# Performance work log

Measured on AMD Instinct MI355X. Metric: run time of the kernel, lower is better.

## Reference

```python
import jax, jax.numpy as jnp
import numpy as np
from jax import lax

B, PN, NS = 8, 16384, 256
KDIM, HID = 512, 384
HALF = HID // 2
EPS = 1e-5


def setup_inputs() -> dict:
    key = jax.random.key(0)
    ks = jax.random.split(key, 12)
    s = lambda fan: np.float32(1.0 / np.sqrt(fan))
    inp = {
        "p": jax.random.normal(ks[0], (B, PN, 3), jnp.float32),
        "N": NS,
        "patch_feature": jax.random.normal(ks[1], (B, KDIM, 1), jnp.float32),
        # Linear(k_dim, hidden)
        "W_feat": jax.random.normal(ks[2], (KDIM, HID), jnp.float32) * s(KDIM),
        "b_feat": jax.random.normal(ks[3], (HID,), jnp.float32) * s(KDIM),
        # Linear(3, hidden//2)
        "W_coord": jax.random.normal(ks[4], (3, HALF), jnp.float32) * s(3),
        "b_coord": jax.random.normal(ks[5], (HALF,), jnp.float32) * s(3),
        # Conv1d(hidden+hidden//2, hidden, 1) == per-point linear, weight (out,in)
        "W1": jax.random.normal(ks[6], (HID, HID + HALF), jnp.float32) * s(HID + HALF),
        "b1": jax.random.normal(ks[7], (HID,), jnp.float32) * s(HID + HALF),
        "g1": jnp.ones((HID,), jnp.float32),
        "be1": jnp.zeros((HID,), jnp.float32),
        # Conv1d(hidden, hidden, 1)
        "W2": jax.random.normal(ks[8], (HID, HID), jnp.float32) * s(HID),
        "b2": jax.random.normal(ks[9], (HID,), jnp.float32) * s(HID),
        "g2": jnp.ones((HID,), jnp.float32),
        "be2": jnp.zeros((HID,), jnp.float32),
    }
    return inp


def farthest_point_sample(points, k):
    """points: (B, N, C) -> (B, k, C). Deterministic start index 0 per batch."""
    b, n, c = points.shape

    def step(carry, _):
        dist, far = carry
        centroid = jnp.take_along_axis(points, far[:, None, None], axis=1)  # (B,1,C)
        d = jnp.sum((points - centroid) ** 2, axis=-1)                      # (B,N)
        dist = jnp.minimum(dist, d)
        new_far = jnp.argmax(dist, axis=-1)
        return (dist, new_far), far

    init = (jnp.full((b, n), 1e10, points.dtype), jnp.zeros((b,), jnp.int32))
    _, idx = lax.scan(step, init, None, length=k)  # idx: (k, B)
    idx = idx.T                                    # (B, k)
    return jnp.take_along_axis(points, idx[:, :, None], axis=1)  # (B,k,C)


def batchnorm(x, gamma, beta):
    """x: (B, L, C); training-mode BN over (B, L) per channel (biased var)."""
    mean = jnp.mean(x, axis=(0, 1))
    var = jnp.var(x, axis=(0, 1))
    return (x - mean) * lax.rsqrt(var + EPS) * gamma + beta


def reference(p, N, patch_feature, W_feat, b_feat, W_coord, b_coord,
              W1, b1, g1, be1, W2, b2, g2, be2):
    b, pn, _ = p.shape
    global_feat = patch_feature[..., 0] @ W_feat + b_feat          # (B, HID)
    global_feat = jnp.broadcast_to(global_feat[:, None, :], (b, N, HID))
    local_feat = p @ W_coord + b_coord                              # (B, PN, HALF)
    if N != pn:
        local_feat = farthest_point_sample(local_feat, N)           # (B, N, HALF)
    combined = jnp.concatenate([global_feat, local_feat], axis=-1)  # (B, N, HID+HALF)
    h = jnp.einsum("bnc,oc->bno", combined, W1) + b1
    h = jax.nn.relu(batchnorm(h, g1, be1))
    h = jnp.einsum("bnc,oc->bno", h, W2) + b2
    h = jax.nn.relu(batchnorm(h, g2, be2))
    return h  # (B, N, HID)
```

## Files before the change

### kernel.cpp

```cpp
#include <hip/hip_runtime.h>

#define BATCH 8
#define PN    16384
#define NSAMP 256
#define KDIM  512
#define HID   384
#define HALF  192
#define CIN   576
#define ROWS  2048
#define BN_EPS 1e-5f

#define OFF_GF   0
#define OFF_W1T  3072
#define OFF_W2T  224256
#define OFF_IDX  371712
#define OFF_H1   373760
#define OFF_H2   1160192
#define OFF_SUM1 1946624
#define OFF_SQ1  1947008
#define OFF_SUM2 1947392
#define OFF_SQ2  1947776

typedef float v2f __attribute__((ext_vector_type(2)));

__device__ __forceinline__ v2f dist2_pk(v2f qx, v2f qy, v2f qz,
                                        v2f cx, v2f cy, v2f cz) {
  v2f dx, dy, dz, d;
  asm("v_pk_add_f32 %0, %4, %7 neg_lo:[0,1] neg_hi:[0,1]\n\t"
      "v_pk_add_f32 %1, %5, %8 neg_lo:[0,1] neg_hi:[0,1]\n\t"
      "v_pk_add_f32 %2, %6, %9 neg_lo:[0,1] neg_hi:[0,1]\n\t"
      "v_pk_mul_f32 %3, %2, %2\n\t"
      "v_pk_fma_f32 %3, %1, %1, %3\n\t"
      "v_pk_fma_f32 %3, %0, %0, %3"
      : "=&v"(dx), "=&v"(dy), "=&v"(dz), "=&v"(d)
      : "v"(qx), "v"(qy), "v"(qz), "v"(cx), "v"(cy), "v"(cz));
  return d;
}

#define DPP_MAX(v, ctrl)                                                   \
  v = fmaxf(v, __int_as_float(__builtin_amdgcn_update_dpp(                 \
          0, __float_as_int(v), (ctrl), 0xf, 0xf, true)))

__global__ __launch_bounds__(1024) void k_main(const float* p, const float* Wc,
                                               const float* pf, const float* Wf,
                                               const float* bfe, const float* W1,
                                               const float* W2, float* ws) {
  __shared__ float s[KDIM];
  __shared__ float Msh[6];
  __shared__ __align__(16) float redv[2][16];
  __shared__ __align__(16) float4 cslot[2][8];
  __shared__ int widx[2], ncl[2];
  int blk = blockIdx.x, t = threadIdx.x;

  if (blk >= 8) {
    if (blk < 16) {
      for (int sI = (blk - 8) * 1024 + t; sI < HID * CIN; sI += 8192) {
        int o = sI / CIN, c = sI % CIN;
        ws[OFF_W1T + c * HID + o] = W1[sI];
      }
    } else if (blk < 24) {
      for (int sI = (blk - 16) * 1024 + t; sI < HID * HID; sI += 8192) {
        int o = sI / HID, c = sI % HID;
        ws[OFF_W2T + c * HID + o] = W2[sI];
      }
    } else if (blk < 32) {
      int b = blk - 24;
      if (t < KDIM) s[t] = pf[b * KDIM + t];
      __syncthreads();
      if (t < HID) {
        float acc = bfe[t];
        for (int k = 0; k < KDIM; k++) acc = fmaf(s[k], Wf[k * HID + t], acc);
        ws[OFF_GF + b * HID + t] = acc;
      }
    } else {
      for (int i = t; i < 1536; i += 1024) ws[OFF_SUM1 + i] = 0.f;
    }
    return;
  }

  int b = blk;
  int* idx_out = (int*)(ws + OFF_IDX);

  if (t < 64) {
    double g0 = 0, g1 = 0, g2 = 0, g3 = 0, g4 = 0, g5 = 0;
    for (int k = t; k < HALF; k += 64) {
      double w0 = (double)Wc[k];
      double w1 = (double)Wc[HALF + k];
      double w2 = (double)Wc[2 * HALF + k];
      g0 += w0 * w0; g1 += w0 * w1; g2 += w0 * w2;
      g3 += w1 * w1; g4 += w1 * w2; g5 += w2 * w2;
    }
    for (int off = 32; off; off >>= 1) {
      g0 += __shfl_down(g0, off, 64); g1 += __shfl_down(g1, off, 64);
      g2 += __shfl_down(g2, off, 64); g3 += __shfl_down(g3, off, 64);
      g4 += __shfl_down(g4, off, 64); g5 += __shfl_down(g5, off, 64);
    }
    if (t == 0) {
      double l00 = sqrt(g0);
      double l10 = g1 / l00, l20 = g2 / l00;
      double l11 = sqrt(g3 - l10 * l10);
      double l21 = (g4 - l10 * l20) / l11;
      double l22 = sqrt(g5 - l20 * l20 - l21 * l21);
      Msh[0] = (float)l00; Msh[1] = (float)l10; Msh[2] = (float)l20;
      Msh[3] = (float)l11; Msh[4] = (float)l21; Msh[5] = (float)l22;
    }
  }
  __syncthreads();
  float m00 = Msh[0], m10 = Msh[1], m20 = Msh[2];
  float m11 = Msh[3], m21 = Msh[4], m22 = Msh[5];

  const float* pb = p + b * PN * 3;
  v2f qx[8], qy[8], qz[8], dist[8];
#pragma unroll
  for (int j = 0; j < 8; j++) {
    int i0 = ((2 * j) << 10) + t;
    int i1 = i0 + 1024;
    float x0 = pb[i0 * 3], y0 = pb[i0 * 3 + 1], z0 = pb[i0 * 3 + 2];
    float x1 = pb[i1 * 3], y1 = pb[i1 * 3 + 1], z1 = pb[i1 * 3 + 2];
    qx[j] = (v2f){fmaf(m00, x0, fmaf(m10, y0, m20 * z0)),
                  fmaf(m00, x1, fmaf(m10, y1, m20 * z1))};
    qy[j] = (v2f){fmaf(m11, y0, m21 * z0), fmaf(m11, y1, m21 * z1)};
    qz[j] = (v2f){m22 * z0, m22 * z1};
    dist[j] = (v2f){1e10f, 1e10f};
  }

  if (t == 0) {
    widx[1] = 0; ncl[1] = 1;
    cslot[1][0] = make_float4(__int_as_float(0), qx[0].x, qy[0].x, qz[0].x);
    widx[0] = 0x7fffffff; ncl[0] = 0;
  }
  __syncthreads();

  int par = 0;
  for (int k = 0; k < NSAMP; k++) {
    int qb = par ^ 1;
    int far = widx[qb];
    float4 s0 = cslot[qb][0];
    float cx = s0.y, cy = s0.z, cz = s0.w;
    if (__float_as_int(s0.x) != far) {
      int n = ncl[qb];
      bool found = false;
      int nn = n < 8 ? n : 8;
      for (int i2 = 1; i2 < nn; i2++) {
        float4 si = cslot[qb][i2];
        if (__float_as_int(si.x) == far) {
          cx = si.y; cy = si.z; cz = si.w; found = true;
        }
      }
      if (!found) {
        float x = pb[far * 3], y = pb[far * 3 + 1], z = pb[far * 3 + 2];
        cx = fmaf(m00, x, fmaf(m10, y, m20 * z));
        cy = fmaf(m11, y, m21 * z);
        cz = m22 * z;
      }
    }
    if (t == 0) {
      idx_out[b * NSAMP + k] = far;
      widx[par] = 0x7fffffff;
      ncl[par] = 0;
    }

    v2f cxv = (v2f){cx, cx}, cyv = (v2f){cy, cy}, czv = (v2f){cz, cz};
#pragma unroll
    for (int j = 0; j < 8; j++) {
      v2f d = dist2_pk(qx[j], qy[j], qz[j], cxv, cyv, czv);
      dist[j].x = fminf(dist[j].x, d.x);
      dist[j].y = fminf(dist[j].y, d.y);
    }
    float a0 = fmaxf(dist[0].x, dist[0].y);
    float a1 = fmaxf(dist[1].x, dist[1].y);
    float a2 = fmaxf(dist[2].x, dist[2].y);
    float a3 = fmaxf(dist[3].x, dist[3].y);
    float a4 = fmaxf(dist[4].x, dist[4].y);
    float a5 = fmaxf(dist[5].x, dist[5].y);
    float a6 = fmaxf(dist[6].x, dist[6].y);
    float a7 = fmaxf(dist[7].x, dist[7].y);
    float b0 = fmaxf(fmaxf(a0, a1), a2);
    float b1 = fmaxf(fmaxf(a3, a4), a5);
    float tmax = fmaxf(fmaxf(b0, b1), fmaxf(a6, a7));
    float wv = tmax;
    DPP_MAX(wv, 0x111);
    DPP_MAX(wv, 0x112);
    DPP_MAX(wv, 0x114);
    DPP_MAX(wv, 0x118);
    DPP_MAX(wv, 0x142);
    DPP_MAX(wv, 0x143);
    if ((t & 63) == 63) redv[par][t >> 6] = wv;
    __syncthreads();
    float4 r0 = *(const float4*)&redv[par][0];
    float4 r1 = *(const float4*)&redv[par][4];
    float4 r2 = *(const float4*)&redv[par][8];
    float4 r3 = *(const float4*)&redv[par][12];
    float g01 = fmaxf(fmaxf(r0.x, r0.y), r0.z);
    float g02 = fmaxf(fmaxf(r0.w, r1.x), r1.y);
    float g03 = fmaxf(fmaxf(r1.z, r1.w), r2.x);
    float g04 = fmaxf(fmaxf(r2.y, r2.z), r2.w);
    float g05 = fmaxf(fmaxf(r3.x, r3.y), r3.z);
    float gmax = fmaxf(fmaxf(fmaxf(g01, g02), g03),
                       fmaxf(fmaxf(g04, g05), r3.w));
    if (tmax == gmax) {
      int mi = 0x7fffffff; float wx = 0.f, wy = 0.f, wz = 0.f;
#pragma unroll
      for (int j = 7; j >= 0; j--) {
        int i0 = ((2 * j) << 10) + t;
        bool hy = (dist[j].y == gmax);
        mi = hy ? i0 + 1024 : mi;
        wx = hy ? qx[j].y : wx; wy = hy ? qy[j].y : wy; wz = hy ? qz[j].y : wz;
        bool hx = (dist[j].x == gmax);
        mi = hx ? i0 : mi;
        wx = hx ? qx[j].x : wx; wy = hx ? qy[j].x : wy; wz = hx ? qz[j].x : wz;
      }
      int pos = atomicAdd(&ncl[par], 1);
      if (pos < 8)
        cslot[par][pos] = make_float4(__int_as_float(mi), wx, wy, wz);
      atomicMin(&widx[par], mi);
    }
    __syncthreads();
    par ^= 1;
  }
}

__global__ __launch_bounds__(384) void k_gemm1(const float* p,
                                               const float* Wc,
                                               const float* bc,
                                               const float* b1,
                                               float* ws) {
  __shared__ __align__(16) float ct[CIN * 8];
  int t = threadIdx.x;
  int row0 = blockIdx.x * 8;
  const int* fidx = (const int*)(ws + OFF_IDX);
  for (int sI = t; sI < 8 * CIN; sI += 384) {
    int r = sI / CIN, c = sI % CIN;
    int row = row0 + r, b = row >> 8;
    float val;
    if (c < HID) {
      val = ws[OFF_GF + b * HID + c];
    } else {
      int co = c - HID;
      int i = fidx[row];
      const float* pp = p + (b * PN + i) * 3;
      val = bc[co];
      val = fmaf(pp[0], Wc[co], val);
      val = fmaf(pp[1], Wc[HALF + co], val);
      val = fmaf(pp[2], Wc[2 * HALF + co], val);
    }
    ct[c * 8 + r] = val;
  }
  __syncthreads();
  const float* w1t = ws + OFF_W1T;
  float acc[8] = {0.f, 0.f, 0.f, 0.f, 0.f, 0.f, 0.f, 0.f};
  for (int c = 0; c < CIN; c++) {
    float w = w1t[c * HID + t];
    float4 a0 = *(const float4*)(ct + c * 8);
    float4 a1 = *(const float4*)(ct + c * 8 + 4);
    acc[0] = fmaf(a0.x, w, acc[0]); acc[1] = fmaf(a0.y, w, acc[1]);
    acc[2] = fmaf(a0.z, w, acc[2]); acc[3] = fmaf(a0.w, w, acc[3]);
    acc[4] = fmaf(a1.x, w, acc[4]); acc[5] = fmaf(a1.y, w, acc[5]);
    acc[6] = fmaf(a1.z, w, acc[6]); acc[7] = fmaf(a1.w, w, acc[7]);
  }
  float bias = b1[t];
  float sv = 0.f, sq = 0.f;
#pragma unroll
  for (int r = 0; r < 8; r++) {
    float v = acc[r] + bias;
    ws[OFF_H1 + (row0 + r) * HID + t] = v;
    sv += v; sq = fmaf(v, v, sq);
  }
  atomicAdd(&ws[OFF_SUM1 + t], sv);
  atomicAdd(&ws[OFF_SQ1 + t], sq);
}

__global__ __launch_bounds__(384) void k_gemm2(const float* b2,
                                               const float* g1,
                                               const float* be1,
                                               float* ws) {
  __shared__ __align__(16) float ht[HID * 8];
  __shared__ float sc1s[HID], sh1s[HID];
  int t = threadIdx.x;
  int row0 = blockIdx.x * 8;
  {
    float m = ws[OFF_SUM1 + t] * (1.f / ROWS);
    float v = ws[OFF_SQ1 + t] * (1.f / ROWS) - m * m;
    float inv = 1.f / sqrtf(v + BN_EPS);
    float sc = inv * g1[t];
    sc1s[t] = sc;
    sh1s[t] = be1[t] - m * sc;
  }
  __syncthreads();
  for (int sI = t; sI < 8 * HID; sI += 384) {
    int r = sI / HID, c = sI % HID;
    float x = fmaf(ws[OFF_H1 + (row0 + r) * HID + c], sc1s[c], sh1s[c]);
    ht[c * 8 + r] = fmaxf(x, 0.f);
  }
  __syncthreads();
  const float* w2t = ws + OFF_W2T;
  float acc[8] = {0.f, 0.f, 0.f, 0.f, 0.f, 0.f, 0.f, 0.f};
  for (int c = 0; c < HID; c++) {
    float w = w2t[c * HID + t];
    float4 a0 = *(const float4*)(ht + c * 8);
    float4 a1 = *(const float4*)(ht + c * 8 + 4);
    acc[0] = fmaf(a0.x, w, acc[0]); acc[1] = fmaf(a0.y, w, acc[1]);
    acc[2] = fmaf(a0.z, w, acc[2]); acc[3] = fmaf(a0.w, w, acc[3]);
    acc[4] = fmaf(a1.x, w, acc[4]); acc[5] = fmaf(a1.y, w, acc[5]);
    acc[6] = fmaf(a1.z, w, acc[6]); acc[7] = fmaf(a1.w, w, acc[7]);
  }
  float bias = b2[t];
  float sv = 0.f, sq = 0.f;
#pragma unroll
  for (int r = 0; r < 8; r++) {
    float v = acc[r] + bias;
    ws[OFF_H2 + (row0 + r) * HID + t] = v;
    sv += v; sq = fmaf(v, v, sq);
  }
  atomicAdd(&ws[OFF_SUM2 + t], sv);
  atomicAdd(&ws[OFF_SQ2 + t], sq);
}

__global__ __launch_bounds__(256) void k_out(const float* ws, const float* g2,
                                             const float* be2, float* out) {
  int gid = blockIdx.x * 256 + threadIdx.x;
  int i = gid * 4;
  int c = i % HID;
  float4 h  = *(const float4*)(ws + OFF_H2 + i);
  float4 s2 = *(const float4*)(ws + OFF_SUM2 + c);
  float4 q2 = *(const float4*)(ws + OFF_SQ2 + c);
  float4 gv = *(const float4*)(g2 + c);
  float4 bv = *(const float4*)(be2 + c);
  float4 r;
#define BN2(comp) {                                                  \
    float m  = s2.comp * (1.f / ROWS);                               \
    float v  = q2.comp * (1.f / ROWS) - m * m;                       \
    float sc = (1.f / sqrtf(v + BN_EPS)) * gv.comp;                  \
    float sh = bv.comp - m * sc;                                     \
    r.comp = fmaxf(fmaf(h.comp, sc, sh), 0.f); }
  BN2(x) BN2(y) BN2(z) BN2(w)
#undef BN2
  ((float4*)out)[gid] = r;
}

extern "C" void kernel_launch(void* const* d_in, const int* in_sizes, int n_in,
                              void* d_out, int out_size, void* d_ws, size_t ws_size,
                              hipStream_t stream) {
  const float* p   = (const float*)d_in[0];
  const float* pf  = (const float*)d_in[2];
  const float* Wf  = (const float*)d_in[3];
  const float* bfe = (const float*)d_in[4];
  const float* Wc  = (const float*)d_in[5];
  const float* bc  = (const float*)d_in[6];
  const float* W1  = (const float*)d_in[7];
  const float* b1  = (const float*)d_in[8];
  const float* g1  = (const float*)d_in[9];
  const float* be1 = (const float*)d_in[10];
  const float* W2  = (const float*)d_in[11];
  const float* b2  = (const float*)d_in[12];
  const float* g2  = (const float*)d_in[13];
  const float* be2 = (const float*)d_in[14];
  float* ws = (float*)d_ws;

  hipLaunchKernelGGL(k_main,  dim3(33),  dim3(1024), 0, stream,
                     p, Wc, pf, Wf, bfe, W1, W2, ws);
  hipLaunchKernelGGL(k_gemm1, dim3(256), dim3(384), 0, stream, p, Wc, bc, b1, ws);
  hipLaunchKernelGGL(k_gemm2, dim3(256), dim3(384), 0, stream, b2, g1, be1, ws);
  hipLaunchKernelGGL(k_out,   dim3(768), dim3(256), 0, stream,
                     ws, g2, be2, (float*)d_out);
}
```

Before: 561.9 us.

## Precompute per-batch global W1 term, expand FPS distance, use shuffle reduction

The global-feature part of the first conv is constant per batch, so it is folded into a per-batch vector (W1_global·gf + b1) computed in k_main. This shrinks the k_gemm1 reduction from 576 to 192 input channels and transposes only the local half of W1. The FPS distance is rewritten as |q|^2+|c|^2-2q·c with precomputed norms, using FMAs instead of subtract-then-square. The DPP wave max becomes a __shfl_xor butterfly. The expanded distance form can change rounding and thus argmax tie-breaking, which risks selecting different points than the reference.

```diff
diff --git a/kernel.cpp b/kernel.cpp
--- a/kernel.cpp
+++ b/kernel.cpp
@@ -12,6 +12,7 @@
 
 #define OFF_GF   0
 #define OFF_W1T  3072
+#define OFF_GFW  76800
 #define OFF_W2T  224256
 #define OFF_IDX  371712
 #define OFF_H1   373760
@@ -23,28 +24,11 @@
 
 typedef float v2f __attribute__((ext_vector_type(2)));
 
-__device__ __forceinline__ v2f dist2_pk(v2f qx, v2f qy, v2f qz,
-                                        v2f cx, v2f cy, v2f cz) {
-  v2f dx, dy, dz, d;
-  asm("v_pk_add_f32 %0, %4, %7 neg_lo:[0,1] neg_hi:[0,1]\n\t"
-      "v_pk_add_f32 %1, %5, %8 neg_lo:[0,1] neg_hi:[0,1]\n\t"
-      "v_pk_add_f32 %2, %6, %9 neg_lo:[0,1] neg_hi:[0,1]\n\t"
-      "v_pk_mul_f32 %3, %2, %2\n\t"
-      "v_pk_fma_f32 %3, %1, %1, %3\n\t"
-      "v_pk_fma_f32 %3, %0, %0, %3"
-      : "=&v"(dx), "=&v"(dy), "=&v"(dz), "=&v"(d)
-      : "v"(qx), "v"(qy), "v"(qz), "v"(cx), "v"(cy), "v"(cz));
-  return d;
-}
-
-#define DPP_MAX(v, ctrl)                                                   \
-  v = fmaxf(v, __int_as_float(__builtin_amdgcn_update_dpp(                 \
-          0, __float_as_int(v), (ctrl), 0xf, 0xf, true)))
-
 __global__ __launch_bounds__(1024) void k_main(const float* p, const float* Wc,
                                                const float* pf, const float* Wf,
                                                const float* bfe, const float* W1,
-                                               const float* W2, float* ws) {
+                                               const float* b1v, const float* W2,
+                                               float* ws) {
   __shared__ float s[KDIM];
   __shared__ float Msh[6];
   __shared__ __align__(16) float redv[2][16];
@@ -54,9 +38,9 @@
 
   if (blk >= 8) {
     if (blk < 16) {
-      for (int sI = (blk - 8) * 1024 + t; sI < HID * CIN; sI += 8192) {
-        int o = sI / CIN, c = sI % CIN;
-        ws[OFF_W1T + c * HID + o] = W1[sI];
+      for (int sI = (blk - 8) * 1024 + t; sI < HID * HALF; sI += 8192) {
+        int o = sI / HALF, c = sI % HALF;
+        ws[OFF_W1T + c * HID + o] = W1[o * CIN + HID + c];
       }
     } else if (blk < 24) {
       for (int sI = (blk - 16) * 1024 + t; sI < HID * HID; sI += 8192) {
@@ -67,10 +51,20 @@
       int b = blk - 24;
       if (t < KDIM) s[t] = pf[b * KDIM + t];
       __syncthreads();
+      float acc = 0.f;
       if (t < HID) {
-        float acc = bfe[t];
+        acc = bfe[t];
         for (int k = 0; k < KDIM; k++) acc = fmaf(s[k], Wf[k * HID + t], acc);
         ws[OFF_GF + b * HID + t] = acc;
+      }
+      __syncthreads();
+      if (t < HID) s[t] = acc;
+      __syncthreads();
+      if (t < HID) {
+        float g = b1v[t];
+        const float* w1row = W1 + t * CIN;
+        for (int c = 0; c < HID; c++) g = fmaf(s[c], w1row[c], g);
+        ws[OFF_GFW + b * HID + t] = g;
       }
     } else {
       for (int i = t; i < 1536; i += 1024) ws[OFF_SUM1 + i] = 0.f;
@@ -110,7 +104,7 @@
   float m11 = Msh[3], m21 = Msh[4], m22 = Msh[5];
 
   const float* pb = p + b * PN * 3;
-  v2f qx[8], qy[8], qz[8], dist[8];
+  v2f qx[8], qy[8], qz[8], nq[8], dist[8];
 #pragma unroll
   for (int j = 0; j < 8; j++) {
     int i0 = ((2 * j) << 10) + t;
@@ -121,6 +115,9 @@
                   fmaf(m00, x1, fmaf(m10, y1, m20 * z1))};
     qy[j] = (v2f){fmaf(m11, y0, m21 * z0), fmaf(m11, y1, m21 * z1)};
     qz[j] = (v2f){m22 * z0, m22 * z1};
+    nq[j] = __builtin_elementwise_fma(
+        qx[j], qx[j],
+        __builtin_elementwise_fma(qy[j], qy[j], qz[j] * qz[j]));
     dist[j] = (v2f){1e10f, 1e10f};
   }
 
@@ -160,10 +157,17 @@
       ncl[par] = 0;
     }
 
-    v2f cxv = (v2f){cx, cx}, cyv = (v2f){cy, cy}, czv = (v2f){cz, cz};
+    float nc = fmaf(cx, cx, fmaf(cy, cy, cz * cz));
+    float cx2 = -2.f * cx, cy2 = -2.f * cy, cz2 = -2.f * cz;
+    v2f cxv = (v2f){cx2, cx2}, cyv = (v2f){cy2, cy2}, czv = (v2f){cz2, cz2};
+    v2f ncv = (v2f){nc, nc};
 #pragma unroll
     for (int j = 0; j < 8; j++) {
-      v2f d = dist2_pk(qx[j], qy[j], qz[j], cxv, cyv, czv);
+      v2f base = nq[j] + ncv;
+      v2f d = __builtin_elementwise_fma(
+          qx[j], cxv,
+          __builtin_elementwise_fma(qy[j], cyv,
+              __builtin_elementwise_fma(qz[j], czv, base)));
       dist[j].x = fminf(dist[j].x, d.x);
       dist[j].y = fminf(dist[j].y, d.y);
     }
@@ -178,14 +182,10 @@
     float b0 = fmaxf(fmaxf(a0, a1), a2);
     float b1 = fmaxf(fmaxf(a3, a4), a5);
     float tmax = fmaxf(fmaxf(b0, b1), fmaxf(a6, a7));
-    float wv = tmax;
-    DPP_MAX(wv, 0x111);
-    DPP_MAX(wv, 0x112);
-    DPP_MAX(wv, 0x114);
-    DPP_MAX(wv, 0x118);
-    DPP_MAX(wv, 0x142);
-    DPP_MAX(wv, 0x143);
-    if ((t & 63) == 63) redv[par][t >> 6] = wv;
+    float m = tmax;
+#pragma unroll
+    for (int off = 32; off; off >>= 1) m = fmaxf(m, __shfl_xor(m, off, 64));
+    if ((t & 63) == 0) redv[par][t >> 6] = m;
     __syncthreads();
     float4 r0 = *(const float4*)&redv[par][0];
     float4 r1 = *(const float4*)&redv[par][4];
@@ -223,33 +223,27 @@
 __global__ __launch_bounds__(384) void k_gemm1(const float* p,
                                                const float* Wc,
                                                const float* bc,
-                                               const float* b1,
                                                float* ws) {
-  __shared__ __align__(16) float ct[CIN * 8];
+  __shared__ __align__(16) float ct[HALF * 8];
   int t = threadIdx.x;
   int row0 = blockIdx.x * 8;
+  int b = row0 >> 8;
   const int* fidx = (const int*)(ws + OFF_IDX);
-  for (int sI = t; sI < 8 * CIN; sI += 384) {
-    int r = sI / CIN, c = sI % CIN;
-    int row = row0 + r, b = row >> 8;
-    float val;
-    if (c < HID) {
-      val = ws[OFF_GF + b * HID + c];
-    } else {
-      int co = c - HID;
-      int i = fidx[row];
-      const float* pp = p + (b * PN + i) * 3;
-      val = bc[co];
-      val = fmaf(pp[0], Wc[co], val);
-      val = fmaf(pp[1], Wc[HALF + co], val);
-      val = fmaf(pp[2], Wc[2 * HALF + co], val);
-    }
-    ct[c * 8 + r] = val;
+  for (int sI = t; sI < 8 * HALF; sI += 384) {
+    int r = sI / HALF, co = sI % HALF;
+    int row = row0 + r;
+    int i = fidx[row];
+    const float* pp = p + (b * PN + i) * 3;
+    float val = bc[co];
+    val = fmaf(pp[0], Wc[co], val);
+    val = fmaf(pp[1], Wc[HALF + co], val);
+    val = fmaf(pp[2], Wc[2 * HALF + co], val);
+    ct[co * 8 + r] = val;
   }
   __syncthreads();
   const float* w1t = ws + OFF_W1T;
   float acc[8] = {0.f, 0.f, 0.f, 0.f, 0.f, 0.f, 0.f, 0.f};
-  for (int c = 0; c < CIN; c++) {
+  for (int c = 0; c < HALF; c++) {
     float w = w1t[c * HID + t];
     float4 a0 = *(const float4*)(ct + c * 8);
     float4 a1 = *(const float4*)(ct + c * 8 + 4);
@@ -258,11 +252,11 @@
     acc[4] = fmaf(a1.x, w, acc[4]); acc[5] = fmaf(a1.y, w, acc[5]);
     acc[6] = fmaf(a1.z, w, acc[6]); acc[7] = fmaf(a1.w, w, acc[7]);
   }
-  float bias = b1[t];
+  float base = ws[OFF_GFW + b * HID + t];
   float sv = 0.f, sq = 0.f;
 #pragma unroll
   for (int r = 0; r < 8; r++) {
-    float v = acc[r] + bias;
+    float v = acc[r] + base;
     ws[OFF_H1 + (row0 + r) * HID + t] = v;
     sv += v; sq = fmaf(v, v, sq);
   }
@@ -358,8 +352,8 @@
   float* ws = (float*)d_ws;
 
   hipLaunchKernelGGL(k_main,  dim3(33),  dim3(1024), 0, stream,
-                     p, Wc, pf, Wf, bfe, W1, W2, ws);
-  hipLaunchKernelGGL(k_gemm1, dim3(256), dim3(384), 0, stream, p, Wc, bc, b1, ws);
+                     p, Wc, pf, Wf, bfe, W1, b1, W2, ws);
+  hipLaunchKernelGGL(k_gemm1, dim3(256), dim3(384), 0, stream, p, Wc, bc, ws);
   hipLaunchKernelGGL(k_gemm2, dim3(256), dim3(384), 0, stream, b2, g1, be1, ws);
   hipLaunchKernelGGL(k_out,   dim3(768), dim3(256), 0, stream,
                      ws, g2, be2, (float*)d_out);
```

Result: faster. 512.8 us (-8.7%).
